# Kernel optimization log

Measured on AMD Instinct MI355X. Metric: run time of the kernel, lower is better.

Reference implementation:

```python
import jax, jax.numpy as jnp
from jax import lax
import numpy as np

B, SQ, SK, H, NH, KS = 2, 2048, 2048, 1024, 16, 3
D = H // NH  # depth per head = 64


def setup_inputs() -> dict:
    key = jax.random.key(0)
    ks = jax.random.split(key, 10)
    s = 0.02
    return {
        "query_input": jax.random.normal(ks[0], (B, SQ, H), jnp.float32),
        "source_input": jax.random.normal(ks[1], (B, SK, H), jnp.float32),
        "mask": jnp.zeros((B, 1, 1, SK), jnp.float32),
        "Wq": jax.random.normal(ks[2], (KS, H, H), jnp.float32) * s,
        "bq": jnp.zeros((H,), jnp.float32),
        "Wk": jax.random.normal(ks[3], (KS, H, H), jnp.float32) * s,
        "bk": jnp.zeros((H,), jnp.float32),
        "Wv": jax.random.normal(ks[4], (KS, H, H), jnp.float32) * s,
        "bv": jnp.zeros((H,), jnp.float32),
        "Wo": jax.random.normal(ks[5], (H, H), jnp.float32) * s,
        "bo": jnp.zeros((H,), jnp.float32),
    }


def _conv1d_same(x, W, b):
    # x: [B, S, H], W: [KS, H_in, H_out] -> 'same' padded 1D conv
    y = lax.conv_general_dilated(x, W, window_strides=(1,), padding="SAME",
                                 dimension_numbers=("NWC", "WIO", "NWC"))
    return y + b


def _split_heads(x):
    # [B, S, H] -> [B, NH, S, D]
    b, s, _ = x.shape
    return x.reshape(b, s, NH, D).transpose(0, 2, 1, 3)


def reference(query_input, source_input, mask, Wq, bq, Wk, bk, Wv, bv, Wo, bo):
    q = _split_heads(_conv1d_same(query_input, Wq, bq)) * (D ** -0.5)
    k = _split_heads(_conv1d_same(source_input, Wk, bk))
    v = _split_heads(_conv1d_same(source_input, Wv, bv))
    logits = jnp.einsum("bhqd,bhkd->bhqk", q, k) + mask * (-1e9)
    weights = jax.nn.softmax(logits, axis=-1)  # dropout omitted (eval mode)
    attn = jnp.einsum("bhqk,bhkd->bhqd", weights, v)
    attn = attn.transpose(0, 2, 1, 3).reshape(q.shape[0], -1, H)
    return attn @ Wo + bo
```

## Files before the change

kernel.cpp:

```cpp
#include <hip/hip_runtime.h>
#include <stdint.h>

#define B_   2
#define S_   2048
#define H_   1024
#define NH_  16
#define D_   64
#define KC_  3072

typedef __attribute__((ext_vector_type(8))) short  short8;
typedef __attribute__((ext_vector_type(4))) float  floatx4;

typedef __attribute__((address_space(1))) const void gas_void;
typedef __attribute__((address_space(3))) void       las_void;

__device__ __forceinline__ void gld16(const void* g, void* l) {
    __builtin_amdgcn_global_load_lds((gas_void*)g, (las_void*)l, 16, 0, 0);
}

__device__ __forceinline__ unsigned short f2bf(float f) {
    union { float f; unsigned u; } v; v.f = f;
    unsigned r = v.u + 0x7fffu + ((v.u >> 16) & 1u);
    return (unsigned short)(r >> 16);
}

__global__ __launch_bounds__(256) void k_pad_convert(const float* __restrict__ src,
                                                     unsigned short* __restrict__ dst) {
    int gid = blockIdx.x * 256 + threadIdx.x;
    int vid = gid * 4;
    if (vid >= B_ * 2050 * 1024) return;
    int row = vid >> 10;
    int b   = (row >= 2050) ? 1 : 0;
    int r   = row - b * 2050;
    int h   = vid & 1023;
    unsigned short o0 = 0, o1 = 0, o2 = 0, o3 = 0;
    if (r != 0 && r != 2049) {
        const float4 f = *(const float4*)(src + ((b * 2048 + r - 1) << 10) + h);
        o0 = f2bf(f.x); o1 = f2bf(f.y); o2 = f2bf(f.z); o3 = f2bf(f.w);
    }
    ushort4 o; o.x = o0; o.y = o1; o.z = o2; o.w = o3;
    *(ushort4*)(dst + vid) = o;
}

__global__ void k_transpose_bf16(const float* __restrict__ src,
                                 unsigned short* __restrict__ dst, int R, int C) {
    __shared__ float t[32][33];
    int c0 = blockIdx.x * 32, r0 = blockIdx.y * 32;
    int tx = threadIdx.x, ty = threadIdx.y;
#pragma unroll
    for (int k = 0; k < 4; ++k)
        t[ty + k * 8][tx] = src[(long)(r0 + ty + k * 8) * C + c0 + tx];
    __syncthreads();
#pragma unroll
    for (int k = 0; k < 4; ++k)
        dst[(long)(c0 + ty + k * 8) * R + r0 + tx] = f2bf(t[tx][ty + k * 8]);
}

__global__ __launch_bounds__(256) void k_conv_gemm(
    const unsigned short* __restrict__ xq, const unsigned short* __restrict__ xs,
    const unsigned short* __restrict__ Wqt, const unsigned short* __restrict__ Wkt,
    const unsigned short* __restrict__ Wvt,
    const float* __restrict__ bq, const float* __restrict__ bk, const float* __restrict__ bv,
    unsigned short* __restrict__ Qo, unsigned short* __restrict__ Ko,
    unsigned short* __restrict__ Vo) {
    int z = blockIdx.z;
    const unsigned short* X = (z == 0) ? xq : xs;
    const unsigned short* W = (z == 0) ? Wqt : (z == 1 ? Wkt : Wvt);
    const float* bias = (z == 0) ? bq : (z == 1 ? bk : bv);

    __shared__ unsigned short Al[2][128 * 64];
    __shared__ unsigned short Bl[2][128 * 64];

    int n0 = blockIdx.x * 128, m0 = blockIdx.y * 128;
    int b = m0 >> 11;
    int tid = threadIdx.x, lane = tid & 63, w = tid >> 6;
    int quad = lane >> 4, l15 = lane & 15;
    int wm = w >> 1, wn = w & 1;

    floatx4 acc[4][4];
#pragma unroll
    for (int i = 0; i < 4; ++i)
#pragma unroll
        for (int j = 0; j < 4; ++j) acc[i][j] = (floatx4){0.f, 0.f, 0.f, 0.f};

    int arow0 = (m0 + 2 * b) * 1024;

    int eoff[4], aoff[4], boff[4];
#pragma unroll
    for (int it = 0; it < 4; ++it) {
        int e  = (it * 256 + tid) * 8;
        int rl = e >> 6;
        int cp = (e >> 3) & 7;
        int c  = cp ^ (rl & 7);
        eoff[it] = e;
        aoff[it] = arow0 + rl * 1024 + c * 8;
        boff[it] = (n0 + rl) * KC_ + c * 8;
    }

    auto stage = [&](int buf, int k0) {
#pragma unroll
        for (int it = 0; it < 4; ++it) {
            gld16(X + aoff[it] + k0, (char*)Al[buf] + eoff[it] * 2);
            gld16(W + boff[it] + k0, (char*)Bl[buf] + eoff[it] * 2);
        }
    };
    auto compute = [&](int buf) {
#pragma unroll
        for (int kk = 0; kk < 2; ++kk) {
            short8 af[4], bf[4];
#pragma unroll
            for (int i = 0; i < 4; ++i) {
                int m  = wm * 64 + i * 16 + l15;
                int cp = (kk * 4 + quad) ^ (m & 7);
                af[i]  = *(const short8*)(Al[buf] + m * 64 + cp * 8);
            }
#pragma unroll
            for (int j = 0; j < 4; ++j) {
                int n  = wn * 64 + j * 16 + l15;
                int cp = (kk * 4 + quad) ^ (n & 7);
                bf[j]  = *(const short8*)(Bl[buf] + n * 64 + cp * 8);
            }
#pragma unroll
            for (int i = 0; i < 4; ++i)
#pragma unroll
                for (int j = 0; j < 4; ++j)
                    acc[i][j] = __builtin_amdgcn_mfma_f32_16x16x32_bf16(af[i], bf[j], acc[i][j], 0, 0, 0);
        }
    };

    stage(0, 0);
    __syncthreads();
    for (int kt = 0; kt < 48; kt += 2) {
        if (kt + 1 < 48) stage(1, (kt + 1) * 64);
        compute(0);
        __syncthreads();
        if (kt + 2 < 48) stage(0, (kt + 2) * 64);
        compute(1);
        __syncthreads();
    }

#pragma unroll
    for (int j = 0; j < 4; ++j) {
        int n = n0 + wn * 64 + j * 16 + l15;
        float bb = bias[n];
        int nh = n >> 6, d = n & 63;
#pragma unroll
        for (int i = 0; i < 4; ++i) {
            int srow = (m0 & 2047) + wm * 64 + i * 16 + quad * 4;
#pragma unroll
            for (int r = 0; r < 4; ++r) {
                float v = acc[i][j][r] + bb;
                int s = srow + r;
                if (z == 0)
                    Qo[((b * NH_ + nh) * 2048 + s) * 64 + d] = f2bf(v * 0.125f);
                else if (z == 1)
                    Ko[((b * NH_ + nh) * 2048 + s) * 64 + d] = f2bf(v);
                else
                    Vo[((b * NH_ + nh) * 64 + d) * 2048 + s] = f2bf(v);
            }
        }
    }
}

__global__ __launch_bounds__(256) void k_flash(
    const unsigned short* __restrict__ Q, const unsigned short* __restrict__ K,
    const unsigned short* __restrict__ Vt, const float* __restrict__ mask,
    unsigned short* __restrict__ Ao) {
    __shared__ unsigned short Ul[128 * 136];
    __shared__ unsigned short Vl[64 * 128];

    int tid = threadIdx.x, w = tid >> 6, lane = tid & 63;
    int quad = lane >> 4, l15 = lane & 15;
    int bh = blockIdx.y;
    int b = bh >> 4, nh = bh & 15;
    int q0 = blockIdx.x * 128, wq = w * 32;

    short8 qf[2][2];
#pragma unroll
    for (int i = 0; i < 2; ++i)
#pragma unroll
        for (int kk = 0; kk < 2; ++kk)
            qf[i][kk] = *(const short8*)(Q + ((bh * 2048 + q0 + wq + i * 16 + l15) << 6) + kk * 32 + quad * 8);

    floatx4 oacc[2][4];
    float rsum[2][4];
#pragma unroll
    for (int i = 0; i < 2; ++i) {
#pragma unroll
        for (int j = 0; j < 4; ++j) oacc[i][j] = (floatx4){0.f, 0.f, 0.f, 0.f};
#pragma unroll
        for (int r = 0; r < 4; ++r) rsum[i][r] = 0.f;
    }
    const float* maskb = mask + b * S_;

    for (int kt = 0; kt < 16; ++kt) {
        int k0 = kt * 128;
#pragma unroll
        for (int it = 0; it < 4; ++it) {
            int e  = (it * 256 + tid) * 8;
            int kl = e >> 6;
            int c  = ((e >> 3) & 7) ^ (kl & 7);
            gld16(K + (bh * 2048 + k0 + kl) * 64 + c * 8, (char*)Ul + e * 2);
            int dl = e >> 7;
            int cp = (e >> 3) & 15;
            int c2 = (cp & 8) | ((cp ^ dl) & 7);
            gld16(Vt + (bh * 64 + dl) * 2048 + k0 + c2 * 8, (char*)Vl + e * 2);
        }
        __syncthreads();

        floatx4 sacc[2][8];
#pragma unroll
        for (int i = 0; i < 2; ++i)
#pragma unroll
            for (int j = 0; j < 8; ++j) sacc[i][j] = (floatx4){0.f, 0.f, 0.f, 0.f};
#pragma unroll
        for (int j = 0; j < 8; ++j) {
            int kl = j * 16 + l15;
            int cp0 = (0 * 4 + quad) ^ (kl & 7);
            short8 bf0 = *(const short8*)(Ul + kl * 64 + cp0 * 8);
            int cp1 = (1 * 4 + quad) ^ (kl & 7);
            short8 bf1 = *(const short8*)(Ul + kl * 64 + cp1 * 8);
#pragma unroll
            for (int i = 0; i < 2; ++i) {
                sacc[i][j] = __builtin_amdgcn_mfma_f32_16x16x32_bf16(qf[i][0], bf0, sacc[i][j], 0, 0, 0);
                sacc[i][j] = __builtin_amdgcn_mfma_f32_16x16x32_bf16(qf[i][1], bf1, sacc[i][j], 0, 0, 0);
            }
        }
        __syncthreads();

#pragma unroll
        for (int j = 0; j < 8; ++j) {
            float mv = maskb[k0 + j * 16 + l15] * (-1e9f);
#pragma unroll
            for (int i = 0; i < 2; ++i) {
                int row = wq + i * 16 + quad * 4;
#pragma unroll
                for (int r = 0; r < 4; ++r) {
                    float p = __expf(sacc[i][j][r] + mv);
                    rsum[i][r] += p;
                    Ul[(row + r) * 136 + j * 16 + l15] = f2bf(p);
                }
            }
        }

#pragma unroll
        for (int kk = 0; kk < 4; ++kk) {
            short8 af[2], bv4[4];
#pragma unroll
            for (int i = 0; i < 2; ++i)
                af[i] = *(const short8*)(Ul + (wq + i * 16 + l15) * 136 + kk * 32 + quad * 8);
#pragma unroll
            for (int j2 = 0; j2 < 4; ++j2) {
                int dl = j2 * 16 + l15;
                int c  = kk * 4 + quad;
                int cp = (c & 8) | ((c ^ dl) & 7);
                bv4[j2] = *(const short8*)(Vl + dl * 128 + cp * 8);
            }
#pragma unroll
            for (int i = 0; i < 2; ++i)
#pragma unroll
                for (int j2 = 0; j2 < 4; ++j2)
                    oacc[i][j2] = __builtin_amdgcn_mfma_f32_16x16x32_bf16(af[i], bv4[j2], oacc[i][j2], 0, 0, 0);
        }
        __syncthreads();
    }

#pragma unroll
    for (int i = 0; i < 2; ++i)
#pragma unroll
        for (int r = 0; r < 4; ++r) {
            float v = rsum[i][r];
            v += __shfl_xor(v, 1); v += __shfl_xor(v, 2);
            v += __shfl_xor(v, 4); v += __shfl_xor(v, 8);
            rsum[i][r] = 1.0f / v;
        }

#pragma unroll
    for (int i = 0; i < 2; ++i)
#pragma unroll
        for (int j2 = 0; j2 < 4; ++j2)
#pragma unroll
            for (int r = 0; r < 4; ++r) {
                int qrow = q0 + wq + i * 16 + quad * 4 + r;
                int hcol = nh * 64 + j2 * 16 + l15;
                Ao[(b * 2048 + qrow) * 1024 + hcol] = f2bf(oacc[i][j2][r] * rsum[i][r]);
            }
}

__global__ __launch_bounds__(256) void k_proj_gemm(
    const unsigned short* __restrict__ A, const unsigned short* __restrict__ Wt,
    const float* __restrict__ bo, float* __restrict__ out) {
    __shared__ unsigned short Al[2][128 * 64];
    __shared__ unsigned short Bl[2][128 * 64];

    int n0 = blockIdx.x * 128, m0 = blockIdx.y * 128;
    int tid = threadIdx.x, lane = tid & 63, w = tid >> 6;
    int quad = lane >> 4, l15 = lane & 15;
    int wm = w >> 1, wn = w & 1;

    floatx4 acc[4][4];
#pragma unroll
    for (int i = 0; i < 4; ++i)
#pragma unroll
        for (int j = 0; j < 4; ++j) acc[i][j] = (floatx4){0.f, 0.f, 0.f, 0.f};

    int eoff[4], aoff[4], boff[4];
#pragma unroll
    for (int it = 0; it < 4; ++it) {
        int e  = (it * 256 + tid) * 8;
        int rl = e >> 6;
        int c  = ((e >> 3) & 7) ^ (rl & 7);
        eoff[it] = e;
        aoff[it] = (m0 + rl) * 1024 + c * 8;
        boff[it] = (n0 + rl) * 1024 + c * 8;
    }

    auto stage = [&](int buf, int k0) {
#pragma unroll
        for (int it = 0; it < 4; ++it) {
            gld16(A + aoff[it] + k0, (char*)Al[buf] + eoff[it] * 2);
            gld16(Wt + boff[it] + k0, (char*)Bl[buf] + eoff[it] * 2);
        }
    };
    auto compute = [&](int buf) {
#pragma unroll
        for (int kk = 0; kk < 2; ++kk) {
            short8 af[4], bf[4];
#pragma unroll
            for (int i = 0; i < 4; ++i) {
                int m  = wm * 64 + i * 16 + l15;
                int cp = (kk * 4 + quad) ^ (m & 7);
                af[i]  = *(const short8*)(Al[buf] + m * 64 + cp * 8);
            }
#pragma unroll
            for (int j = 0; j < 4; ++j) {
                int n  = wn * 64 + j * 16 + l15;
                int cp = (kk * 4 + quad) ^ (n & 7);
                bf[j]  = *(const short8*)(Bl[buf] + n * 64 + cp * 8);
            }
#pragma unroll
            for (int i = 0; i < 4; ++i)
#pragma unroll
                for (int j = 0; j < 4; ++j)
                    acc[i][j] = __builtin_amdgcn_mfma_f32_16x16x32_bf16(af[i], bf[j], acc[i][j], 0, 0, 0);
        }
    };

    stage(0, 0);
    __syncthreads();
    for (int kt = 0; kt < 16; kt += 2) {
        if (kt + 1 < 16) stage(1, (kt + 1) * 64);
        compute(0);
        __syncthreads();
        if (kt + 2 < 16) stage(0, (kt + 2) * 64);
        compute(1);
        __syncthreads();
    }

#pragma unroll
    for (int j = 0; j < 4; ++j) {
        int n = n0 + wn * 64 + j * 16 + l15;
        float bb = bo[n];
#pragma unroll
        for (int i = 0; i < 4; ++i) {
            int m = m0 + wm * 64 + i * 16 + quad * 4;
#pragma unroll
            for (int r = 0; r < 4; ++r)
                out[(m + r) * 1024 + n] = acc[i][j][r] + bb;
        }
    }
}

extern "C" void kernel_launch(void* const* d_in, const int* in_sizes, int n_in,
                              void* d_out, int out_size, void* d_ws, size_t ws_size,
                              hipStream_t stream) {
    (void)in_sizes; (void)n_in; (void)out_size; (void)ws_size;
    const float* q_in = (const float*)d_in[0];
    const float* s_in = (const float*)d_in[1];
    const float* mask = (const float*)d_in[2];
    const float* Wq   = (const float*)d_in[3];
    const float* bq   = (const float*)d_in[4];
    const float* Wk   = (const float*)d_in[5];
    const float* bk   = (const float*)d_in[6];
    const float* Wv   = (const float*)d_in[7];
    const float* bv   = (const float*)d_in[8];
    const float* Wo   = (const float*)d_in[9];
    const float* bo   = (const float*)d_in[10];
    float* out = (float*)d_out;

    char* ws = (char*)d_ws;
    size_t off = 0;
    auto alloc = [&](size_t bytes) {
        char* p = ws + off;
        off += (bytes + 255) & ~(size_t)255;
        return p;
    };
    unsigned short* xqp = (unsigned short*)alloc((size_t)B_ * 2050 * 1024 * 2);
    unsigned short* xsp = (unsigned short*)alloc((size_t)B_ * 2050 * 1024 * 2);
    unsigned short* Wqt = (unsigned short*)alloc((size_t)KC_ * H_ * 2);
    unsigned short* Wkt = (unsigned short*)alloc((size_t)KC_ * H_ * 2);
    unsigned short* Wvt = (unsigned short*)alloc((size_t)KC_ * H_ * 2);
    unsigned short* Wot = (unsigned short*)alloc((size_t)H_ * H_ * 2);
    unsigned short* Qb  = (unsigned short*)alloc((size_t)B_ * NH_ * S_ * D_ * 2);
    unsigned short* Kb  = (unsigned short*)alloc((size_t)B_ * NH_ * S_ * D_ * 2);
    unsigned short* Vtb = (unsigned short*)alloc((size_t)B_ * NH_ * S_ * D_ * 2);
    unsigned short* Ab  = (unsigned short*)alloc((size_t)B_ * S_ * H_ * 2);

    k_pad_convert<<<4100, 256, 0, stream>>>(q_in, xqp);
    k_pad_convert<<<4100, 256, 0, stream>>>(s_in, xsp);
    k_transpose_bf16<<<dim3(32, 96), dim3(32, 8), 0, stream>>>(Wq, Wqt, KC_, H_);
    k_transpose_bf16<<<dim3(32, 96), dim3(32, 8), 0, stream>>>(Wk, Wkt, KC_, H_);
    k_transpose_bf16<<<dim3(32, 96), dim3(32, 8), 0, stream>>>(Wv, Wvt, KC_, H_);
    k_transpose_bf16<<<dim3(32, 32), dim3(32, 8), 0, stream>>>(Wo, Wot, H_, H_);
    k_conv_gemm<<<dim3(8, 32, 3), 256, 0, stream>>>(xqp, xsp, Wqt, Wkt, Wvt,
                                                    bq, bk, bv, Qb, Kb, Vtb);
    k_flash<<<dim3(16, 32), 256, 0, stream>>>(Qb, Kb, Vtb, mask, Ab);
    k_proj_gemm<<<dim3(8, 32), 256, 0, stream>>>(Ab, Wot, bo, out);
}
```

Before: 361.3 us.

## Fuse prep kernels, reuse conv input rows across taps, halve proj tile

Merges the six pad/convert and weight-transpose launches into one prep kernel to cut launch overhead. The conv GEMM now loads a 130-row input slab once per 32-wide K step and reuses it for all three kernel taps by shifting the row index, instead of reading the padded input separately for each tap. This reduces global traffic for the A operand, but the conv loop is now single-buffered with a sync every iteration. The output projection uses 64-row M tiles, doubling the grid so more blocks are in flight.

```diff
diff --git a/kernel.cpp b/kernel.cpp
--- a/kernel.cpp
+++ b/kernel.cpp
@@ -24,29 +24,48 @@
     return (unsigned short)(r >> 16);
 }
 
-__global__ __launch_bounds__(256) void k_pad_convert(const float* __restrict__ src,
-                                                     unsigned short* __restrict__ dst) {
-    int gid = blockIdx.x * 256 + threadIdx.x;
-    int vid = gid * 4;
-    if (vid >= B_ * 2050 * 1024) return;
-    int row = vid >> 10;
-    int b   = (row >= 2050) ? 1 : 0;
-    int r   = row - b * 2050;
-    int h   = vid & 1023;
-    unsigned short o0 = 0, o1 = 0, o2 = 0, o3 = 0;
-    if (r != 0 && r != 2049) {
-        const float4 f = *(const float4*)(src + ((b * 2048 + r - 1) << 10) + h);
-        o0 = f2bf(f.x); o1 = f2bf(f.y); o2 = f2bf(f.z); o3 = f2bf(f.w);
-    }
-    ushort4 o; o.x = o0; o.y = o1; o.z = o2; o.w = o3;
-    *(ushort4*)(dst + vid) = o;
-}
-
-__global__ void k_transpose_bf16(const float* __restrict__ src,
-                                 unsigned short* __restrict__ dst, int R, int C) {
+__global__ __launch_bounds__(256) void k_prep(
+    const float* __restrict__ qin, const float* __restrict__ sin,
+    const float* __restrict__ Wq, const float* __restrict__ Wk,
+    const float* __restrict__ Wv, const float* __restrict__ Wo,
+    unsigned short* __restrict__ xqp, unsigned short* __restrict__ xsp,
+    unsigned short* __restrict__ Wqt, unsigned short* __restrict__ Wkt,
+    unsigned short* __restrict__ Wvt, unsigned short* __restrict__ Wot) {
+    int bid = blockIdx.x, tid = threadIdx.x;
+    if (bid < 8200) {
+        const float* src = (bid < 4100) ? qin : sin;
+        unsigned short* dst = (bid < 4100) ? xqp : xsp;
+        int b0 = (bid < 4100) ? bid : bid - 4100;
+        int vid = (b0 * 256 + tid) * 4;
+        if (vid >= B_ * 2050 * 1024) return;
+        int row = vid >> 10;
+        int b   = (row >= 2050) ? 1 : 0;
+        int r   = row - b * 2050;
+        int h   = vid & 1023;
+        unsigned short o0 = 0, o1 = 0, o2 = 0, o3 = 0;
+        if (r != 0 && r != 2049) {
+            const float4 f = *(const float4*)(src + ((b * 2048 + r - 1) << 10) + h);
+            o0 = f2bf(f.x); o1 = f2bf(f.y); o2 = f2bf(f.z); o3 = f2bf(f.w);
+        }
+        ushort4 o; o.x = o0; o.y = o1; o.z = o2; o.w = o3;
+        *(ushort4*)(dst + vid) = o;
+        return;
+    }
     __shared__ float t[32][33];
-    int c0 = blockIdx.x * 32, r0 = blockIdx.y * 32;
-    int tx = threadIdx.x, ty = threadIdx.y;
+    const float* src; unsigned short* dst; int R, bx, by;
+    int tbid = bid - 8200;
+    if (tbid < 9216) {
+        int w = tbid / 3072, rem = tbid - w * 3072;
+        src = (w == 0) ? Wq : (w == 1 ? Wk : Wv);
+        dst = (w == 0) ? Wqt : (w == 1 ? Wkt : Wvt);
+        R = 3072; bx = rem & 31; by = rem >> 5;
+    } else {
+        int rem = tbid - 9216;
+        src = Wo; dst = Wot; R = 1024; bx = rem & 31; by = rem >> 5;
+    }
+    const int C = 1024;
+    int c0 = bx * 32, r0 = by * 32;
+    int tx = tid & 31, ty = tid >> 5;
 #pragma unroll
     for (int k = 0; k < 4; ++k)
         t[ty + k * 8][tx] = src[(long)(r0 + ty + k * 8) * C + c0 + tx];
@@ -68,8 +87,8 @@
     const unsigned short* W = (z == 0) ? Wqt : (z == 1 ? Wkt : Wvt);
     const float* bias = (z == 0) ? bq : (z == 1 ? bk : bv);
 
-    __shared__ unsigned short Al[2][128 * 64];
-    __shared__ unsigned short Bl[2][128 * 64];
+    __shared__ unsigned short Al[520 * 8];
+    __shared__ unsigned short Bl[1536 * 8];
 
     int n0 = blockIdx.x * 128, m0 = blockIdx.y * 128;
     int b = m0 >> 11;
@@ -83,42 +102,53 @@
 #pragma unroll
         for (int j = 0; j < 4; ++j) acc[i][j] = (floatx4){0.f, 0.f, 0.f, 0.f};
 
-    int arow0 = (m0 + 2 * b) * 1024;
-
-    int eoff[4], aoff[4], boff[4];
-#pragma unroll
-    for (int it = 0; it < 4; ++it) {
-        int e  = (it * 256 + tid) * 8;
-        int rl = e >> 6;
-        int cp = (e >> 3) & 7;
-        int c  = cp ^ (rl & 7);
-        eoff[it] = e;
-        aoff[it] = arow0 + rl * 1024 + c * 8;
-        boff[it] = (n0 + rl) * KC_ + c * 8;
-    }
-
-    auto stage = [&](int buf, int k0) {
-#pragma unroll
-        for (int it = 0; it < 4; ++it) {
-            gld16(X + aoff[it] + k0, (char*)Al[buf] + eoff[it] * 2);
-            gld16(W + boff[it] + k0, (char*)Bl[buf] + eoff[it] * 2);
-        }
-    };
-    auto compute = [&](int buf) {
-#pragma unroll
-        for (int kk = 0; kk < 2; ++kk) {
+    const unsigned short* Xbase = X + (m0 + 2 * b) * 1024;
+
+    int aoff[3];
+#pragma unroll
+    for (int it = 0; it < 3; ++it) {
+        int s = it * 256 + tid;
+        if (s < 520) {
+            int pr = s >> 3, p = s & 7, u = p ^ (pr & 7);
+            aoff[it] = (pr * 2 + (u >> 2)) * 1024 + (u & 3) * 8;
+        }
+    }
+    int boff[6];
+#pragma unroll
+    for (int it = 0; it < 6; ++it) {
+        int s = it * 256 + tid;
+        int tt = s >> 9, sp = s & 511;
+        int pr = sp >> 3, p = sp & 7, u = p ^ (pr & 7);
+        boff[it] = (n0 + pr * 2 + (u >> 2)) * KC_ + tt * 1024 + (u & 3) * 8;
+    }
+
+    for (int kt = 0; kt < 32; ++kt) {
+        int k0 = kt * 32;
+        gld16(Xbase + aoff[0] + k0, (char*)Al + tid * 16);
+        gld16(Xbase + aoff[1] + k0, (char*)Al + (256 + tid) * 16);
+        if (tid < 8)
+            gld16(Xbase + aoff[2] + k0, (char*)Al + (512 + tid) * 16);
+#pragma unroll
+        for (int it = 0; it < 6; ++it)
+            gld16(W + boff[it] + k0, (char*)Bl + (it * 256 + tid) * 16);
+        __syncthreads();
+
+#pragma unroll
+        for (int t = 0; t < 3; ++t) {
             short8 af[4], bf[4];
 #pragma unroll
             for (int i = 0; i < 4; ++i) {
-                int m  = wm * 64 + i * 16 + l15;
-                int cp = (kk * 4 + quad) ^ (m & 7);
-                af[i]  = *(const short8*)(Al[buf] + m * 64 + cp * 8);
+                int r  = wm * 64 + i * 16 + l15 + t;
+                int pr = r >> 1;
+                int p  = (((r & 1) << 2) | quad) ^ (pr & 7);
+                af[i]  = *(const short8*)(Al + (pr * 8 + p) * 8);
             }
 #pragma unroll
             for (int j = 0; j < 4; ++j) {
                 int n  = wn * 64 + j * 16 + l15;
-                int cp = (kk * 4 + quad) ^ (n & 7);
-                bf[j]  = *(const short8*)(Bl[buf] + n * 64 + cp * 8);
+                int pr = n >> 1;
+                int p  = (((n & 1) << 2) | quad) ^ (pr & 7);
+                bf[j]  = *(const short8*)(Bl + (t * 512 + pr * 8 + p) * 8);
             }
 #pragma unroll
             for (int i = 0; i < 4; ++i)
@@ -126,16 +156,6 @@
                 for (int j = 0; j < 4; ++j)
                     acc[i][j] = __builtin_amdgcn_mfma_f32_16x16x32_bf16(af[i], bf[j], acc[i][j], 0, 0, 0);
         }
-    };
-
-    stage(0, 0);
-    __syncthreads();
-    for (int kt = 0; kt < 48; kt += 2) {
-        if (kt + 1 < 48) stage(1, (kt + 1) * 64);
-        compute(0);
-        __syncthreads();
-        if (kt + 2 < 48) stage(0, (kt + 2) * 64);
-        compute(1);
         __syncthreads();
     }
 
@@ -290,45 +310,53 @@
 __global__ __launch_bounds__(256) void k_proj_gemm(
     const unsigned short* __restrict__ A, const unsigned short* __restrict__ Wt,
     const float* __restrict__ bo, float* __restrict__ out) {
-    __shared__ unsigned short Al[2][128 * 64];
+    __shared__ unsigned short Al[2][64 * 64];
     __shared__ unsigned short Bl[2][128 * 64];
 
-    int n0 = blockIdx.x * 128, m0 = blockIdx.y * 128;
+    int n0 = blockIdx.x * 128, m0 = blockIdx.y * 64;
     int tid = threadIdx.x, lane = tid & 63, w = tid >> 6;
     int quad = lane >> 4, l15 = lane & 15;
     int wm = w >> 1, wn = w & 1;
 
-    floatx4 acc[4][4];
-#pragma unroll
-    for (int i = 0; i < 4; ++i)
+    floatx4 acc[2][4];
+#pragma unroll
+    for (int i = 0; i < 2; ++i)
 #pragma unroll
         for (int j = 0; j < 4; ++j) acc[i][j] = (floatx4){0.f, 0.f, 0.f, 0.f};
 
-    int eoff[4], aoff[4], boff[4];
+    int ea[2], ao[2], eb[4], bof[4];
+#pragma unroll
+    for (int it = 0; it < 2; ++it) {
+        int e  = (it * 256 + tid) * 8;
+        int rl = e >> 6;
+        int c  = ((e >> 3) & 7) ^ (rl & 7);
+        ea[it] = e;
+        ao[it] = (m0 + rl) * 1024 + c * 8;
+    }
 #pragma unroll
     for (int it = 0; it < 4; ++it) {
         int e  = (it * 256 + tid) * 8;
         int rl = e >> 6;
         int c  = ((e >> 3) & 7) ^ (rl & 7);
-        eoff[it] = e;
-        aoff[it] = (m0 + rl) * 1024 + c * 8;
-        boff[it] = (n0 + rl) * 1024 + c * 8;
+        eb[it] = e;
+        bof[it] = (n0 + rl) * 1024 + c * 8;
     }
 
     auto stage = [&](int buf, int k0) {
 #pragma unroll
-        for (int it = 0; it < 4; ++it) {
-            gld16(A + aoff[it] + k0, (char*)Al[buf] + eoff[it] * 2);
-            gld16(Wt + boff[it] + k0, (char*)Bl[buf] + eoff[it] * 2);
-        }
+        for (int it = 0; it < 2; ++it)
+            gld16(A + ao[it] + k0, (char*)Al[buf] + ea[it] * 2);
+#pragma unroll
+        for (int it = 0; it < 4; ++it)
+            gld16(Wt + bof[it] + k0, (char*)Bl[buf] + eb[it] * 2);
     };
     auto compute = [&](int buf) {
 #pragma unroll
         for (int kk = 0; kk < 2; ++kk) {
-            short8 af[4], bf[4];
-#pragma unroll
-            for (int i = 0; i < 4; ++i) {
-                int m  = wm * 64 + i * 16 + l15;
+            short8 af[2], bf[4];
+#pragma unroll
+            for (int i = 0; i < 2; ++i) {
+                int m  = wm * 32 + i * 16 + l15;
                 int cp = (kk * 4 + quad) ^ (m & 7);
                 af[i]  = *(const short8*)(Al[buf] + m * 64 + cp * 8);
             }
@@ -339,7 +367,7 @@
                 bf[j]  = *(const short8*)(Bl[buf] + n * 64 + cp * 8);
             }
 #pragma unroll
-            for (int i = 0; i < 4; ++i)
+            for (int i = 0; i < 2; ++i)
 #pragma unroll
                 for (int j = 0; j < 4; ++j)
                     acc[i][j] = __builtin_amdgcn_mfma_f32_16x16x32_bf16(af[i], bf[j], acc[i][j], 0, 0, 0);
@@ -362,8 +390,8 @@
         int n = n0 + wn * 64 + j * 16 + l15;
         float bb = bo[n];
 #pragma unroll
-        for (int i = 0; i < 4; ++i) {
-            int m = m0 + wm * 64 + i * 16 + quad * 4;
+        for (int i = 0; i < 2; ++i) {
+            int m = m0 + wm * 32 + i * 16 + quad * 4;
 #pragma unroll
             for (int r = 0; r < 4; ++r)
                 out[(m + r) * 1024 + n] = acc[i][j][r] + bb;
@@ -406,14 +434,10 @@
     unsigned short* Vtb = (unsigned short*)alloc((size_t)B_ * NH_ * S_ * D_ * 2);
     unsigned short* Ab  = (unsigned short*)alloc((size_t)B_ * S_ * H_ * 2);
 
-    k_pad_convert<<<4100, 256, 0, stream>>>(q_in, xqp);
-    k_pad_convert<<<4100, 256, 0, stream>>>(s_in, xsp);
-    k_transpose_bf16<<<dim3(32, 96), dim3(32, 8), 0, stream>>>(Wq, Wqt, KC_, H_);
-    k_transpose_bf16<<<dim3(32, 96), dim3(32, 8), 0, stream>>>(Wk, Wkt, KC_, H_);
-    k_transpose_bf16<<<dim3(32, 96), dim3(32, 8), 0, stream>>>(Wv, Wvt, KC_, H_);
-    k_transpose_bf16<<<dim3(32, 32), dim3(32, 8), 0, stream>>>(Wo, Wot, H_, H_);
+    k_prep<<<18440, 256, 0, stream>>>(q_in, s_in, Wq, Wk, Wv, Wo,
+                                      xqp, xsp, Wqt, Wkt, Wvt, Wot);
     k_conv_gemm<<<dim3(8, 32, 3), 256, 0, stream>>>(xqp, xsp, Wqt, Wkt, Wvt,
                                                     bq, bk, bv, Qb, Kb, Vtb);
     k_flash<<<dim3(16, 32), 256, 0, stream>>>(Qb, Kb, Vtb, mask, Ab);
-    k_proj_gemm<<<dim3(8, 32), 256, 0, stream>>>(Ab, Wot, bo, out);
-}
+    k_proj_gemm<<<dim3(8, 64), 256, 0, stream>>>(Ab, Wot, bo, out);
+}
```

Measured after the change: 325.4 us. 1.11x faster.
